# Kernel optimization log

Hardware: AMD Instinct MI355X
Metric: run time of the kernel (lower is better)

## Reference

```python
import jax, jax.numpy as jnp
import numpy as np

G = 4            # GroupNorm num_groups
EPS_GN = 1e-3    # GroupNorm eps
TEMP = 1.0
SCALE = 4.0      # sqrt(prod(out_ks)) with out_ks=(4,4)
OUT_CL = 8


def group_norm(x):
    # torch GroupNorm(4, d, affine=False) applied on (b, d, n*t): stats per (sample, group)
    b, n, t, d = x.shape
    xr = x.reshape(b, n * t, G, d // G)
    mu = xr.mean(axis=(1, 3), keepdims=True)
    var = xr.var(axis=(1, 3), keepdims=True)
    return ((xr - mu) * jax.lax.rsqrt(var + EPS_GN)).reshape(b, n, t, d)


def mlp(x, W1, b1, W2, b2):
    return jax.nn.leaky_relu(x @ W1 + b1) @ W2 + b2


def sq_dist(x, y):
    # squared euclidean distance, expansion form (avoids [.., nq, nk, d] intermediate)
    x2 = jnp.sum(x * x, axis=-1)
    y2 = jnp.sum(y * y, axis=-1)
    return x2[..., :, None] + y2[..., None, :] - 2.0 * jnp.einsum('...qd,...kd->...qk', x, y)


def clamp_pg(x, lo, hi):
    # clamp_preserve_gradients
    return x + jax.lax.stop_gradient(jnp.clip(x, lo, hi) - x)


def min_pair_tril_sum(d, a):
    # sum_{i<j} 2*min(d_i,d_j)*a_i*a_j along last axis.
    # Identical value to the original tril(diagonal=-1)-masked [.., n, n] reduction,
    # computed via sort + suffix-sum in O(n log n) without the 5-D intermediate.
    order = jnp.argsort(d, axis=-1)
    ds = jnp.take_along_axis(d, order, axis=-1)
    as_ = jnp.take_along_axis(a, order, axis=-1)
    suffix = jnp.flip(jnp.cumsum(jnp.flip(as_, -1), axis=-1), -1) - as_
    return jnp.sum(2.0 * ds * as_ * suffix, axis=-1, keepdims=True)


def calc_compactness(mask, in_dens, in_area, in_iner, qcor, kcor):
    densT = jnp.swapaxes(in_dens, -1, -2)
    areaT = jnp.swapaxes(in_area, -1, -2)
    inerT = jnp.swapaxes(in_iner, -1, -2)
    d = mask * densT           # (b, nw, nq, nk)
    a = mask * areaT
    m = d * a
    i = d * inerT
    dist = sq_dist(qcor, kcor)
    newiner = jnp.sum(i, -1, keepdims=True) + jnp.sum(m * dist, -1, keepdims=True)
    refiner = (jnp.sum(m * a, -1, keepdims=True) + min_pair_tril_sum(d, a)) / (2.0 * np.pi)
    return refiner / newiner, newiner


def cluster(af, dens, area, iner, coor, eps=1e-8):
    b, nw, nqn, nkn = af.shape
    af = clamp_pg(af, 1e-5, 0.99999)
    comp, _ = calc_compactness(af, dens, area, iner, coor, coor)   # (b, nw, nqn, 1)
    log_sc = jnp.zeros((b, nw, 1, nkn), af.dtype)
    log_cl, cl_rs = [], []
    for _ in range(OUT_CL - 1):   # small fixed iteration count (greedy cluster picks)
        score = comp[..., 0] * jnp.exp(log_sc)[:, :, 0, :]          # (b, nw, nqn)
        idx = jnp.argmax(score, axis=-1)                            # (b, nw)
        row = jnp.take_along_axis(af, jnp.broadcast_to(idx[:, :, None, None], (b, nw, 1, nkn)), axis=-2)
        log_cl.append(log_sc + jnp.log(row))
        log_sc = log_sc + jnp.log(1.0 - row)
        cl_rs.append(idx)
    sc_lm = jnp.exp(log_sc)                                         # (b, nw, 1, nkn)
    cl_r = jnp.stack(cl_rs, axis=-1)[..., None]                     # (b, nw, OUT_CL-1, 1)
    cl_m = jnp.concatenate([jnp.exp(jnp.concatenate(log_cl, axis=-2)), sc_lm], axis=-2)  # (b,nw,OUT_CL,nkn)
    densT = jnp.swapaxes(dens, -1, -2)
    areaT = jnp.swapaxes(area, -1, -2)
    cd = cl_m * densT
    ca = cl_m * areaT
    cm = cd * ca
    cl_coor = jnp.einsum('bwck,bwkd->bwcd', cm, coor) / (jnp.sum(cm, -1, keepdims=True) + eps)
    cl_area = jnp.sum(ca, -1, keepdims=True)
    cl_mass = jnp.sum(cm, -1, keepdims=True)
    cl_dens = cl_mass / (cl_area + eps)
    cl_comp, cl_iner = calc_compactness(cl_m, dens, area, iner, cl_coor, coor)
    return cl_m, cl_dens, cl_mass, cl_area, cl_iner, cl_coor, cl_comp, cl_r, sc_lm


def setup_inputs() -> dict:
    key = jax.random.key(0)
    ks = jax.random.split(key, 12)
    b, nw, nn, d = 8, 256, 64, 128
    s = 1.0 / np.sqrt(d)
    return {
        'in_f': jax.random.normal(ks[0], (b, nw, nn, d), jnp.float32),
        'in_geo': jax.random.uniform(ks[1], (b, nw, nn, 6), jnp.float32),
        'W1': jax.random.normal(ks[2], (d, d), jnp.float32) * s,
        'b1': jnp.full((d,), 0.1, jnp.float32),
        'W2': jax.random.normal(ks[3], (d, d), jnp.float32) * s,
        'b2': jnp.full((d,), 0.1, jnp.float32),
        'Wfc': jax.random.normal(ks[4], (d, d), jnp.float32) * s,
        'bfc': jnp.zeros((d,), jnp.float32),
        'Wq': jax.random.normal(ks[5], (d, d), jnp.float32) * s,
        'Wv': jax.random.normal(ks[6], (d, d), jnp.float32) * s,
    }


def reference(in_f, in_geo, W1, b1, W2, b2, Wfc, bfc, Wq, Wv):
    dens = in_geo[..., 0:1]
    area = in_geo[..., 2:3]
    iner = in_geo[..., 3:4]
    coor = in_geo[..., 4:6]
    _f = group_norm(in_f)
    f_m = mlp(_f, W1, b1, W2, b2)
    f_v = _f @ Wv
    q = group_norm(_f @ Wq)                                      # to_cl
    scl = TEMP / SCALE / np.sqrt(q.shape[-1])
    af = jax.nn.softmax(-scl * sq_dist(q, q), axis=-1)           # softmin of scaled sq-dists
    af_max = jnp.max(af, -1, keepdims=True)
    af_min = jnp.min(af, -1, keepdims=True)
    af = (af - af_min) / (af_max - af_min + 1e-8)
    (cl_m, cl_dens, cl_mass, cl_area, cl_iner, cl_coor, cl_comp, cl_r, sc_m) = cluster(af, dens, area, iner, coor)
    cl_mm = cl_m / (jnp.sum(cl_m, -1, keepdims=True) + 1e-8)
    cl_f = jnp.einsum('bwck,bwkd->bwcd', cl_mm, in_f)
    cl_f = cl_f + jnp.einsum('bwck,bwkd->bwcd', cl_mm, f_m) + (jnp.einsum('bwck,bwkd->bwcd', cl_mm, f_v) @ Wfc + bfc)
    cl_geo = jnp.concatenate([cl_dens, cl_mass, cl_area, cl_iner, cl_coor], axis=-1)
    return cl_f, cl_m, cl_geo, cl_r, cl_comp, af, sc_m, q
```

## Files before the change

### kernel.cpp

```cpp
#include <hip/hip_runtime.h>

#define TWO_PI_F 6.28318530717958647692f
#define SCL_F    0.02209708691207961f

typedef __attribute__((ext_vector_type(8))) short s16x8;
typedef __attribute__((ext_vector_type(4))) float f32x4;

__device__ __forceinline__ float rlane(float v, int l) {
    return __uint_as_float((unsigned)__builtin_amdgcn_readlane((int)__float_as_uint(v), l));
}

__device__ __forceinline__ unsigned short f2bf(float f) {
    unsigned u = __float_as_uint(f);
    return (unsigned short)((u + 0x7fff + ((u >> 16) & 1)) >> 16);
}
__device__ __forceinline__ float bf2f(unsigned short h) {
    return __uint_as_float(((unsigned)h) << 16);
}

__global__ __launch_bounds__(256) void gn_partial_k(const float* __restrict__ X,
                                                    float* __restrict__ partials)
{
    int t = threadIdx.x;
    int chunk = blockIdx.x;
    int grp = blockIdx.y;
    int b = grp >> 2, g = grp & 3;
    const float* base = X + ((long)b * 16384 + (long)chunk * 256) * 128 + g * 32;
    float s = 0.f, ss = 0.f;
#pragma unroll
    for (int i = 0; i < 8; i++) {
        int rl_ = i * 32 + (t >> 3);
        int c4 = (t & 7) * 4;
        float4 v = *(const float4*)(base + (long)rl_ * 128 + c4);
        s  += v.x + v.y + v.z + v.w;
        ss += v.x * v.x + v.y * v.y + v.z * v.z + v.w * v.w;
    }
    __shared__ float r0[256], r1[256];
    r0[t] = s; r1[t] = ss;
    __syncthreads();
    for (int off = 128; off > 0; off >>= 1) {
        if (t < off) { r0[t] += r0[t + off]; r1[t] += r1[t + off]; }
        __syncthreads();
    }
    if (t == 0) {
        partials[(grp * 64 + chunk) * 2]     = r0[0];
        partials[(grp * 64 + chunk) * 2 + 1] = r1[0];
    }
}

__global__ void gn_final_k(const float* __restrict__ partials, float* __restrict__ stats,
                           int nblk)
{
    int grp = blockIdx.x, t = threadIdx.x;
    float s = 0.f, ss = 0.f;
    for (int i = t; i < nblk; i += 64) {
        s  += partials[(grp * nblk + i) * 2];
        ss += partials[(grp * nblk + i) * 2 + 1];
    }
    for (int off = 1; off < 64; off <<= 1) { s += __shfl_xor(s, off); ss += __shfl_xor(ss, off); }
    if (t == 0) {
        const float N = 524288.0f;
        float mu = s / N;
        float var = ss / N - mu * mu;
        stats[grp * 2]     = mu;
        stats[grp * 2 + 1] = 1.0f / sqrtf(var + 0.001f);
    }
}

__global__ __launch_bounds__(256) void wvf_prep_k(const float* __restrict__ Wv,
                                                  const float* __restrict__ Wfc,
                                                  float* __restrict__ out)
{
    int t = threadIdx.x;
    int rr = t >> 6, cl = t & 63;
    int r = blockIdx.x * 4 + rr;
    float a0 = 0.f, a1 = 0.f;
    for (int k = 0; k < 128; k++) {
        float wv = Wv[r * 128 + k];
        a0 = fmaf(wv, Wfc[k * 128 + cl], a0);
        a1 = fmaf(wv, Wfc[k * 128 + 64 + cl], a1);
    }
    out[r * 128 + cl] = a0;
    out[r * 128 + 64 + cl] = a1;
}

__global__ __launch_bounds__(256) void wsplit_prep_k(const float* __restrict__ W1,
                                                     const float* __restrict__ Wq,
                                                     unsigned short* __restrict__ WThi,
                                                     unsigned short* __restrict__ WTlo)
{
    int idx = blockIdx.x * 256 + threadIdx.x;
    int col = idx >> 7, k = idx & 127;
    float w = (col < 128) ? W1[k * 128 + col] : Wq[k * 128 + (col - 128)];
    unsigned short hb = f2bf(w);
    float hf = bf2f(hb);
    WThi[col * 128 + k] = hb;
    WTlo[col * 128 + k] = f2bf(w - hf);
}

__global__ __launch_bounds__(512, 4) void gemm_mfma_dual(const float* __restrict__ X,
                                                         const unsigned short* __restrict__ WThi,
                                                         const unsigned short* __restrict__ WTlo,
                                                         const float* __restrict__ b1,
                                                         const float* __restrict__ stats,
                                                         float* __restrict__ C1,
                                                         float* __restrict__ C2,
                                                         float* __restrict__ statsout)
{
    __shared__ short sAhi[128 * 40];
    __shared__ short sAlo[128 * 40];
    __shared__ short sBhi[256 * 40];
    __shared__ short sBlo[256 * 40];
    int t = threadIdx.x;
    int wv = t >> 6, lane = t & 63;
    int half = wv >> 2;
    int mrow0 = (wv & 3) * 32;
    long row0 = (long)blockIdx.x * 128;
    int bidx = (int)(row0 >> 14);

    float muv[4], rsv[4];
#pragma unroll
    for (int g = 0; g < 4; g++) {
        muv[g] = stats[(bidx * 4 + g) * 2];
        rsv[g] = stats[(bidx * 4 + g) * 2 + 1];
    }

    f32x4 acc[2][8];
#pragma unroll
    for (int m2 = 0; m2 < 2; m2++)
#pragma unroll
        for (int nt = 0; nt < 8; nt++) acc[m2][nt] = (f32x4){0.f, 0.f, 0.f, 0.f};

    int lr = lane & 15, lk = (lane >> 4) * 8;
    int arow = t >> 2, akq = (t & 3) * 8;
    int bcol = t >> 1, bko = (t & 1) * 16;
    const float* xsrc = X + (row0 + arow) * 128;

    for (int kt = 0; kt < 4; kt++) {
        {
            float mu = muv[kt], rs = rsv[kt];
            float4 x0 = *(const float4*)(xsrc + kt * 32 + akq);
            float4 x1 = *(const float4*)(xsrc + kt * 32 + akq + 4);
            float v[8];
            v[0] = x0.x; v[1] = x0.y; v[2] = x0.z; v[3] = x0.w;
            v[4] = x1.x; v[5] = x1.y; v[6] = x1.z; v[7] = x1.w;
            s16x8 vh, vl;
#pragma unroll
            for (int j = 0; j < 8; j++) {
                float x = (v[j] - mu) * rs;
                unsigned short hb = f2bf(x);
                float hf = bf2f(hb);
                unsigned short lb = f2bf(x - hf);
                vh[j] = (short)hb;
                vl[j] = (short)lb;
            }
            *(s16x8*)&sAhi[arow * 40 + akq] = vh;
            *(s16x8*)&sAlo[arow * 40 + akq] = vl;
        }
        {
            const unsigned short* sh = WThi + bcol * 128 + kt * 32 + bko;
            const unsigned short* sl = WTlo + bcol * 128 + kt * 32 + bko;
            *(s16x8*)&sBhi[bcol * 40 + bko]     = *(const s16x8*)(sh);
            *(s16x8*)&sBhi[bcol * 40 + bko + 8] = *(const s16x8*)(sh + 8);
            *(s16x8*)&sBlo[bcol * 40 + bko]     = *(const s16x8*)(sl);
            *(s16x8*)&sBlo[bcol * 40 + bko + 8] = *(const s16x8*)(sl + 8);
        }
        __syncthreads();
        s16x8 ahi[2], alo[2];
#pragma unroll
        for (int m2 = 0; m2 < 2; m2++) {
            int row = mrow0 + m2 * 16 + lr;
            ahi[m2] = *(const s16x8*)&sAhi[row * 40 + lk];
            alo[m2] = *(const s16x8*)&sAlo[row * 40 + lk];
        }
#pragma unroll
        for (int nt = 0; nt < 8; nt++) {
            int col = half * 128 + nt * 16 + lr;
            s16x8 bhi = *(const s16x8*)&sBhi[col * 40 + lk];
            s16x8 blo = *(const s16x8*)&sBlo[col * 40 + lk];
#pragma unroll
            for (int m2 = 0; m2 < 2; m2++) {
                acc[m2][nt] = __builtin_amdgcn_mfma_f32_16x16x32_bf16(ahi[m2], bhi, acc[m2][nt], 0, 0, 0);
                acc[m2][nt] = __builtin_amdgcn_mfma_f32_16x16x32_bf16(alo[m2], bhi, acc[m2][nt], 0, 0, 0);
                acc[m2][nt] = __builtin_amdgcn_mfma_f32_16x16x32_bf16(ahi[m2], blo, acc[m2][nt], 0, 0, 0);
            }
        }
        __syncthreads();
    }

    int rg4 = (lane >> 4) * 4;
    float* C = half ? C2 : C1;
    float bv[8];
    if (half == 0) {
#pragma unroll
        for (int nt = 0; nt < 8; nt++) bv[nt] = b1[nt * 16 + lr];
    }
#pragma unroll
    for (int m2 = 0; m2 < 2; m2++) {
        long rbase = row0 + mrow0 + m2 * 16 + rg4;
#pragma unroll
        for (int nt = 0; nt < 8; nt++) {
#pragma unroll
            for (int r = 0; r < 4; r++) {
                float v = acc[m2][nt][r];
                if (half == 0) {
                    v += bv[nt];
                    v = (v >= 0.f) ? v : 0.01f * v;
                }
                C[(rbase + r) * 128 + nt * 16 + lr] = v;
            }
        }
    }
    float s4[4] = {0.f, 0.f, 0.f, 0.f}, ss4[4] = {0.f, 0.f, 0.f, 0.f};
    if (half == 1) {
#pragma unroll
        for (int m2 = 0; m2 < 2; m2++)
#pragma unroll
            for (int nt = 0; nt < 8; nt++) {
                int g = nt >> 1;
#pragma unroll
                for (int r = 0; r < 4; r++) {
                    float v = acc[m2][nt][r];
                    s4[g] += v; ss4[g] += v * v;
                }
            }
    }
    __syncthreads();
    float* sRed = (float*)sAhi;
    if (half == 1) {
        int q = t & 255;
#pragma unroll
        for (int g = 0; g < 4; g++) {
            sRed[q * 8 + 2 * g]     = s4[g];
            sRed[q * 8 + 2 * g + 1] = ss4[g];
        }
    }
    __syncthreads();
    if (t < 8) {
        int g = t >> 1, which = t & 1;
        float a2 = 0.f;
        for (int u = 0; u < 256; u++) a2 += sRed[u * 8 + 2 * g + which];
        statsout[((bidx * 4 + g) * 128 + (int)(blockIdx.x & 127)) * 2 + which] = a2;
    }
}

__global__ __launch_bounds__(256, 2) void attn_v2(const float* __restrict__ Qraw,
                                                  const float* __restrict__ stats,
                                                  float* __restrict__ outQ,
                                                  float* __restrict__ outAF)
{
    __shared__ float sQ[2][8192];
    __shared__ float sN[2][64];
    int t = threadIdx.x;
    int wl = t >> 7;
    int tl = t & 127;
    int w = blockIdx.x * 2 + wl;
    int bidx = w >> 8;
    float muv[4], rsv[4];
#pragma unroll
    for (int g = 0; g < 4; g++) {
        muv[g] = stats[(bidx * 4 + g) * 2];
        rsv[g] = stats[(bidx * 4 + g) * 2 + 1];
    }
    {
        int r = tl >> 1, q0 = (tl & 1) * 16;
        int sw = r >> 3;
        const float* src = Qraw + (long)w * 8192 + r * 128 + q0 * 4;
        float* dstG = outQ + (long)w * 8192 + r * 128 + q0 * 4;
#pragma unroll
        for (int q = 0; q < 16; q++) {
            float4 v = *(const float4*)(src + 4 * q);
            int g = (q0 + q) >> 3;
            float mu = muv[g], rs = rsv[g];
            v.x = (v.x - mu) * rs; v.y = (v.y - mu) * rs;
            v.z = (v.z - mu) * rs; v.w = (v.w - mu) * rs;
            *(float4*)(dstG + 4 * q) = v;
            *(float4*)&sQ[wl][r * 128 + 4 * ((q0 + q) ^ sw)] = v;
        }
    }
    __syncthreads();
    if (tl < 64) {
        int r = tl, sw = r >> 3;
        float s = 0.f;
#pragma unroll
        for (int q = 0; q < 32; q++) {
            float4 v = *(const float4*)&sQ[wl][r * 128 + 4 * (q ^ sw)];
            s += v.x * v.x + v.y * v.y + v.z * v.z + v.w * v.w;
        }
        sN[wl][r] = s;
    }
    __syncthreads();
    int ty = tl >> 4, tx = tl & 15;
    float acc[8][4];
#pragma unroll
    for (int i = 0; i < 8; i++)
#pragma unroll
        for (int bb = 0; bb < 4; bb++) acc[i][bb] = 0.f;
    for (int kq = 0; kq < 32; kq++) {
        float4 bf[4];
#pragma unroll
        for (int bb = 0; bb < 4; bb++) {
            int col = tx * 4 + bb;
            bf[bb] = *(const float4*)&sQ[wl][col * 128 + 4 * (kq ^ (col >> 3))];
        }
#pragma unroll
        for (int i = 0; i < 8; i++) {
            int row = ty * 8 + i;
            float4 av = *(const float4*)&sQ[wl][row * 128 + 4 * (kq ^ (row >> 3))];
#pragma unroll
            for (int bb = 0; bb < 4; bb++)
                acc[i][bb] += av.x * bf[bb].x + av.y * bf[bb].y
                            + av.z * bf[bb].z + av.w * bf[bb].w;
        }
    }
    __syncthreads();
    float* sS = &sQ[wl][0];
#pragma unroll
    for (int i = 0; i < 8; i++) {
        int row = ty * 8 + i;
#pragma unroll
        for (int bb = 0; bb < 4; bb++) {
            int col = tx * 4 + bb;
            sS[row * 65 + col] = sN[wl][row] + sN[wl][col] - 2.f * acc[i][bb];
        }
    }
    __syncthreads();
    if (tl < 64) {
        int r = tl;
        float mnS = sS[r * 65];
        for (int j = 1; j < 64; j++) mnS = fminf(mnS, sS[r * 65 + j]);
        float sum = 0.f, pmx = -1.f, pmn = 1e30f;
        for (int j = 0; j < 64; j++) {
            float p = expf(-SCL_F * (sS[r * 65 + j] - mnS));
            sS[r * 65 + j] = p;
            sum += p;
            pmx = fmaxf(pmx, p);
            pmn = fminf(pmn, p);
        }
        float rsum = 1.0f / sum;
        float amn = pmn * rsum, amx = pmx * rsum;
        float dinv = 1.0f / (amx - amn + 1e-8f);
        float* dst = outAF + (long)w * 4096 + r * 64;
        for (int j = 0; j < 64; j += 4) {
            float4 o;
            o.x = (sS[r * 65 + j + 0] * rsum - amn) * dinv;
            o.y = (sS[r * 65 + j + 1] * rsum - amn) * dinv;
            o.z = (sS[r * 65 + j + 2] * rsum - amn) * dinv;
            o.w = (sS[r * 65 + j + 3] * rsum - amn) * dinv;
            *(float4*)(dst + j) = o;
        }
    }
}

__global__ __launch_bounds__(256, 4) void cluster_v3(const float* __restrict__ AF,
                                                     const float* __restrict__ GEO,
                                                     float* __restrict__ oCLM,
                                                     float* __restrict__ oCLR,
                                                     float* __restrict__ oCOMP,
                                                     float* __restrict__ oGEO,
                                                     float* __restrict__ oSCM,
                                                     float* __restrict__ wCLMM)
{
    __shared__ float sAF[64 * 65];
    __shared__ float sPart[4 * 64 * 3];
    __shared__ float sCLM[8 * 65];
    int t = threadIdx.x, w = blockIdx.x;
    int wv = t >> 6, lane = t & 63;
    const float* afw = AF + (long)w * 4096;
#pragma unroll
    for (int i = 0; i < 4; i++) {
        int f4 = i * 256 + t;
        float4 v = *(const float4*)(afw + f4 * 4);
        int r = f4 >> 4, c4 = (f4 & 15) * 4;
        float* dst = &sAF[r * 65 + c4];
        dst[0] = fminf(fmaxf(v.x, 1e-5f), 0.99999f);
        dst[1] = fminf(fmaxf(v.y, 1e-5f), 0.99999f);
        dst[2] = fminf(fmaxf(v.z, 1e-5f), 0.99999f);
        dst[3] = fminf(fmaxf(v.w, 1e-5f), 0.99999f);
    }
    const float* gp = GEO + ((long)w * 64 + lane) * 6;
    float2 g01 = *(const float2*)(gp);
    float2 g23 = *(const float2*)(gp + 2);
    float2 g45 = *(const float2*)(gp + 4);
    float gD = g01.x, gA = g23.x, gI = g23.y, gX = g45.x, gY = g45.y;
    __syncthreads();

    const float* afrow = &sAF[lane * 65];
    float dk[16], ak[16], T[16];
    float v0 = 0.f, v1 = 0.f;
#pragma unroll
    for (int kk = 0; kk < 16; kk++) {
        int kc = kk * 4 + wv;
        float afk = afrow[kc];
        float d = afk * rlane(gD, kc);
        float a = afk * rlane(gA, kc);
        dk[kk] = d; ak[kk] = a; T[kk] = 0.f;
        float m = d * a;
        float dx = gX - rlane(gX, kc), dy = gY - rlane(gY, kc);
        v0 += d * rlane(gI, kc) + m * (dx * dx + dy * dy);
        v1 += m * a;
    }
    for (int jq = 0; jq < 16; jq++) {
        float dj[4], aj[4];
#pragma unroll
        for (int jr = 0; jr < 4; jr++) {
            int j = jq * 4 + jr;
            float afj = afrow[j];
            dj[jr] = afj * rlane(gD, j);
            aj[jr] = afj * rlane(gA, j);
        }
#pragma unroll
        for (int kk = 0; kk < 16; kk++) {
            if (kk > jq) {
#pragma unroll
                for (int jr = 0; jr < 4; jr++)
                    T[kk] = fmaf(aj[jr], fminf(dj[jr], dk[kk]), T[kk]);
            } else if (kk == jq) {
                if (0 < wv) T[kk] = fmaf(aj[0], fminf(dj[0], dk[kk]), T[kk]);
                if (1 < wv) T[kk] = fmaf(aj[1], fminf(dj[1], dk[kk]), T[kk]);
                if (2 < wv) T[kk] = fmaf(aj[2], fminf(dj[2], dk[kk]), T[kk]);
            }
        }
    }
    float S = 0.f;
#pragma unroll
    for (int kk = 0; kk < 16; kk++) S = fmaf(ak[kk], T[kk], S);
    {
        float* p = &sPart[(wv * 64 + lane) * 3];
        p[0] = v0; p[1] = v1; p[2] = S;
    }
    __syncthreads();

    if (t < 64) {
        int k = lane;
        float c0 = 0.f, c1 = 0.f, c2 = 0.f;
#pragma unroll
        for (int u = 0; u < 4; u++) {
            const float* p = &sPart[(u * 64 + k) * 3];
            c0 += p[0]; c1 += p[1]; c2 += p[2];
        }
        float compk = ((c1 + 2.f * c2) / TWO_PI_F) / c0;
        float sc = 1.0f;
        for (int c = 0; c < 7; c++) {
            float score = compk * sc;
            float mx = score;
            for (int off = 1; off < 64; off <<= 1) mx = fmaxf(mx, __shfl_xor(mx, off));
            unsigned long long bl = __ballot(score == mx);
            int idx = __ffsll(bl) - 1;
            float rowk = sAF[idx * 65 + k];
            float clm = sc * rowk;
            sCLM[c * 65 + k] = clm;
            oCLM[(long)w * 512 + c * 64 + k] = clm;
            if (k == 0) oCLR[(long)w * 7 + c] = (float)idx;
            sc *= (1.0f - rowk);
        }
        sCLM[7 * 65 + k] = sc;
        oCLM[(long)w * 512 + 448 + k] = sc;
        oSCM[(long)w * 64 + k] = sc;
    }
    __syncthreads();

    {
        int k = lane;
        for (int cc = 0; cc < 2; cc++) {
            int c = wv + cc * 4;
            float clm = sCLM[c * 65 + k];
            float cd = clm * gD, ca = clm * gA;
            float cm = cd * ca;
            float T3 = 0.f;
            for (int j = 0; j < 64; j++)
                T3 = fmaf(rlane(ca, j), fminf(rlane(cd, j), cd), T3);
            float r0 = cm, r1 = ca, r2c = cm * gX, r3 = cm * gY, r4 = clm;
            float r5 = cm * ca;
            float r6 = ca * T3 - ca * ca * cd;
            for (int off = 1; off < 64; off <<= 1) {
                r0 += __shfl_xor(r0, off); r1 += __shfl_xor(r1, off);
                r2c += __shfl_xor(r2c, off); r3 += __shfl_xor(r3, off);
                r4 += __shfl_xor(r4, off); r5 += __shfl_xor(r5, off);
                r6 += __shfl_xor(r6, off);
            }
            float mass = r0, area = r1;
            float qx = r2c / (mass + 1e-8f), qy = r3 / (mass + 1e-8f);
            wCLMM[(long)w * 512 + c * 64 + k] = clm / (r4 + 1e-8f);
            float dx = qx - gX, dy = qy - gY;
            float w0v = cd * gI + cm * (dx * dx + dy * dy);
            for (int off = 1; off < 64; off <<= 1) w0v += __shfl_xor(w0v, off);
            if (k == 0) {
                oCOMP[(long)w * 8 + c] = ((r5 + r6) / TWO_PI_F) / w0v;
                float* og = oGEO + (long)w * 48 + c * 6;
                og[0] = mass / (area + 1e-8f); og[1] = mass; og[2] = area;
                og[3] = w0v; og[4] = qx; og[5] = qy;
            }
        }
    }
}

__global__ __launch_bounds__(256, 4) void final_v3(const float* __restrict__ inF,
                                                   const float* __restrict__ H1,
                                                   const float* __restrict__ CLMM,
                                                   const float* __restrict__ stats1,
                                                   const float* __restrict__ W2,
                                                   const float* __restrict__ b2,
                                                   const float* __restrict__ Wvf,
                                                   const float* __restrict__ bfc,
                                                   float* __restrict__ oCLF)
{
    __shared__ float sU[8 * 129];
    __shared__ float sT[8 * 129];
    __shared__ float sP[8 * 129];
    int t = threadIdx.x, w = blockIdx.x;
    int bidx = w >> 8;
    int wv = t >> 6, lane = t & 63;
    int ch = lane + 64 * (wv & 1);

    float mmL[8];
#pragma unroll
    for (int c = 0; c < 8; c++)
        mmL[c] = CLMM[(long)w * 512 + c * 64 + lane];

    float mu = stats1[(bidx * 4 + (ch >> 5)) * 2];
    float rs = stats1[(bidx * 4 + (ch >> 5)) * 2 + 1];

    float acc1[8];
#pragma unroll
    for (int c = 0; c < 8; c++) acc1[c] = 0.f;
    if (wv < 2) {
        const float* src = H1 + (long)w * 8192 + ch;
#pragma unroll 4
        for (int j = 0; j < 64; j++) {
            float f = src[j * 128];
#pragma unroll
            for (int c = 0; c < 8; c++)
                acc1[c] = fmaf(rlane(mmL[c], j), f, acc1[c]);
        }
#pragma unroll
        for (int c = 0; c < 8; c++) sU[c * 129 + ch] = acc1[c];
    } else {
        const float* src = inF + (long)w * 8192 + ch;
#pragma unroll 4
        for (int j = 0; j < 64; j++) {
            float f = (src[j * 128] - mu) * rs;
#pragma unroll
            for (int c = 0; c < 8; c++)
                acc1[c] = fmaf(rlane(mmL[c], j), f, acc1[c]);
        }
#pragma unroll
        for (int c = 0; c < 8; c++) sT[c * 129 + ch] = acc1[c];
    }
    __syncthreads();
    float xL0[8], xL1[8];
    {
        const float* s2 = (wv < 2) ? sU : sT;
#pragma unroll
        for (int c = 0; c < 8; c++) {
            xL0[c] = s2[c * 129 + lane];
            xL1[c] = s2[c * 129 + 64 + lane];
        }
    }
    const float* Wm = (wv < 2) ? W2 : Wvf;
    float acc2[8];
#pragma unroll
    for (int c = 0; c < 8; c++) acc2[c] = 0.f;
#pragma unroll 2
    for (int k = 0; k < 64; k++) {
        float wk = Wm[k * 128 + ch];
#pragma unroll
        for (int c = 0; c < 8; c++)
            acc2[c] = fmaf(rlane(xL0[c], k), wk, acc2[c]);
    }
#pragma unroll 2
    for (int k = 0; k < 64; k++) {
        float wk = Wm[(k + 64) * 128 + ch];
#pragma unroll
        for (int c = 0; c < 8; c++)
            acc2[c] = fmaf(rlane(xL1[c], k), wk, acc2[c]);
    }
    if (wv >= 2) {
        float sig = 1.0f / rs;
#pragma unroll
        for (int c = 0; c < 8; c++) {
            float t1ch = (wv & 1) ? xL1[c] : xL0[c];
            acc2[c] = fmaf(t1ch, sig, acc2[c]);
        }
#pragma unroll
        for (int c = 0; c < 8; c++) sP[c * 129 + ch] = acc2[c];
    }
    __syncthreads();
    if (wv < 2) {
        float scv[8];
#pragma unroll
        for (int c = 0; c < 8; c++) {
            float s = mmL[c];
            for (int off = 1; off < 64; off <<= 1) s += __shfl_xor(s, off);
            scv[c] = s;
        }
        float mub = mu + b2[ch];
        float bfv = bfc[ch];
#pragma unroll
        for (int c = 0; c < 8; c++) {
            float o = acc2[c] + sP[c * 129 + ch] + scv[c] * mub + bfv;
            oCLF[(long)w * 1024 + c * 128 + ch] = o;
        }
    }
}

extern "C" void kernel_launch(void* const* d_in, const int* in_sizes, int n_in,
                              void* d_out, int out_size, void* d_ws, size_t ws_size,
                              hipStream_t stream)
{
    (void)in_sizes; (void)n_in; (void)out_size; (void)ws_size;
    const float* in_f   = (const float*)d_in[0];
    const float* in_geo = (const float*)d_in[1];
    const float* W1  = (const float*)d_in[2];
    const float* b1  = (const float*)d_in[3];
    const float* W2  = (const float*)d_in[4];
    const float* b2  = (const float*)d_in[5];
    const float* Wfc = (const float*)d_in[6];
    const float* bfc = (const float*)d_in[7];
    const float* Wq  = (const float*)d_in[8];
    const float* Wv  = (const float*)d_in[9];
    float* out = (float*)d_out;
    float* ws  = (float*)d_ws;

    float* qh     = ws;
    float* clmm   = ws + 16777216;
    float* stats1 = ws + 17825792;
    float* stats2 = ws + 17825856;
    float* wvf    = ws + 17825920;
    float* part   = ws + 17842304;

    unsigned short* wthi = (unsigned short*)clmm;
    unsigned short* wtlo = ((unsigned short*)clmm) + 32768;

    float* o_clf  = out;
    float* o_clm  = out + 2097152;
    float* o_geo  = out + 3145728;
    float* o_clr  = out + 3244032;
    float* o_comp = out + 3258368;
    float* o_af   = out + 3274752;
    float* o_scm  = out + 11663360;
    float* o_q    = out + 11794432;

    gn_partial_k<<<dim3(64, 32), 256, 0, stream>>>(in_f, part);
    gn_final_k<<<32, 64, 0, stream>>>(part, stats1, 64);
    wvf_prep_k<<<32, 256, 0, stream>>>(Wv, Wfc, wvf);
    wsplit_prep_k<<<128, 256, 0, stream>>>(W1, Wq, wthi, wtlo);
    gemm_mfma_dual<<<1024, 512, 0, stream>>>(in_f, wthi, wtlo, b1, stats1, qh, o_q, part);
    gn_final_k<<<32, 64, 0, stream>>>(part, stats2, 128);
    attn_v2<<<1024, 256, 0, stream>>>(o_q, stats2, o_q, o_af);
    cluster_v3<<<2048, 256, 0, stream>>>(o_af, in_geo, o_clm, o_clr, o_comp, o_geo,
                                         o_scm, clmm);
    final_v3<<<2048, 256, 0, stream>>>(in_f, qh, clmm, stats1, W2, b2, wvf, bfc, o_clf);
}
```

Before: 394.4 us.

## Rewrite attention kernel with split-bf16 MFMA Gram and parallel softmin

Replaces the FP32 scalar Gram-matrix computation in the attention kernel with bf16 MFMA instructions. Each value is split into a hi and a lo bf16 part and three products are accumulated to keep near-fp32 accuracy. Each block now handles one window with four wavefronts, and the row normalisation and softmin work is spread over four threads per row using shuffles, where only 64 of 128 threads were busy before. The smaller LDS footprint allows three blocks per CU, at the cost of some added precision error from the bf16 split and extra conversion work.

```diff
diff --git a/kernel.cpp b/kernel.cpp
--- a/kernel.cpp
+++ b/kernel.cpp
@@ -244,110 +244,131 @@
     }
 }
 
-__global__ __launch_bounds__(256, 2) void attn_v2(const float* __restrict__ Qraw,
+__global__ __launch_bounds__(256, 3) void attn_v3(const float* __restrict__ Qraw,
                                                   const float* __restrict__ stats,
                                                   float* __restrict__ outQ,
                                                   float* __restrict__ outAF)
 {
-    __shared__ float sQ[2][8192];
-    __shared__ float sN[2][64];
+    __shared__ short sYhi[4 * 64 * 40];
+    __shared__ short sYlo[4 * 64 * 40];
+    __shared__ float sN[64];
+    float* sS = (float*)sYlo;
     int t = threadIdx.x;
-    int wl = t >> 7;
-    int tl = t & 127;
-    int w = blockIdx.x * 2 + wl;
+    int wv = t >> 6, lane = t & 63;
+    int w = blockIdx.x;
     int bidx = w >> 8;
-    float muv[4], rsv[4];
-#pragma unroll
-    for (int g = 0; g < 4; g++) {
-        muv[g] = stats[(bidx * 4 + g) * 2];
-        rsv[g] = stats[(bidx * 4 + g) * 2 + 1];
-    }
+
     {
-        int r = tl >> 1, q0 = (tl & 1) * 16;
-        int sw = r >> 3;
-        const float* src = Qraw + (long)w * 8192 + r * 128 + q0 * 4;
-        float* dstG = outQ + (long)w * 8192 + r * 128 + q0 * 4;
-#pragma unroll
-        for (int q = 0; q < 16; q++) {
-            float4 v = *(const float4*)(src + 4 * q);
-            int g = (q0 + q) >> 3;
-            float mu = muv[g], rs = rsv[g];
-            v.x = (v.x - mu) * rs; v.y = (v.y - mu) * rs;
-            v.z = (v.z - mu) * rs; v.w = (v.w - mu) * rs;
-            *(float4*)(dstG + 4 * q) = v;
-            *(float4*)&sQ[wl][r * 128 + 4 * ((q0 + q) ^ sw)] = v;
-        }
-    }
-    __syncthreads();
-    if (tl < 64) {
-        int r = tl, sw = r >> 3;
-        float s = 0.f;
-#pragma unroll
-        for (int q = 0; q < 32; q++) {
-            float4 v = *(const float4*)&sQ[wl][r * 128 + 4 * (q ^ sw)];
-            s += v.x * v.x + v.y * v.y + v.z * v.z + v.w * v.w;
-        }
-        sN[wl][r] = s;
-    }
-    __syncthreads();
-    int ty = tl >> 4, tx = tl & 15;
-    float acc[8][4];
-#pragma unroll
-    for (int i = 0; i < 8; i++)
-#pragma unroll
-        for (int bb = 0; bb < 4; bb++) acc[i][bb] = 0.f;
-    for (int kq = 0; kq < 32; kq++) {
-        float4 bf[4];
-#pragma unroll
-        for (int bb = 0; bb < 4; bb++) {
-            int col = tx * 4 + bb;
-            bf[bb] = *(const float4*)&sQ[wl][col * 128 + 4 * (kq ^ (col >> 3))];
-        }
-#pragma unroll
-        for (int i = 0; i < 8; i++) {
-            int row = ty * 8 + i;
-            float4 av = *(const float4*)&sQ[wl][row * 128 + 4 * (kq ^ (row >> 3))];
-#pragma unroll
-            for (int bb = 0; bb < 4; bb++)
-                acc[i][bb] += av.x * bf[bb].x + av.y * bf[bb].y
-                            + av.z * bf[bb].z + av.w * bf[bb].w;
-        }
-    }
-    __syncthreads();
-    float* sS = &sQ[wl][0];
-#pragma unroll
-    for (int i = 0; i < 8; i++) {
-        int row = ty * 8 + i;
-#pragma unroll
-        for (int bb = 0; bb < 4; bb++) {
-            int col = tx * 4 + bb;
-            sS[row * 65 + col] = sN[wl][row] + sN[wl][col] - 2.f * acc[i][bb];
-        }
-    }
-    __syncthreads();
-    if (tl < 64) {
-        int r = tl;
-        float mnS = sS[r * 65];
-        for (int j = 1; j < 64; j++) mnS = fminf(mnS, sS[r * 65 + j]);
+        int row = t >> 2, kc = t & 3;
+        float mu = stats[(bidx * 4 + kc) * 2];
+        float rs = stats[(bidx * 4 + kc) * 2 + 1];
+        const float* src = Qraw + (long)w * 8192 + row * 128 + kc * 32;
+        float* dstG = outQ + (long)w * 8192 + row * 128 + kc * 32;
+        s16x8 vh[4], vl[4];
+        float n = 0.f;
+#pragma unroll
+        for (int q4 = 0; q4 < 8; q4++) {
+            float4 v = *(const float4*)(src + 4 * q4);
+            float vv[4] = {v.x, v.y, v.z, v.w};
+            float4 o;
+#pragma unroll
+            for (int e = 0; e < 4; e++) {
+                float x = (vv[e] - mu) * rs;
+                (&o.x)[e] = x;
+                n += x * x;
+                unsigned short hb = f2bf(x);
+                float hf = bf2f(hb);
+                int kk = q4 * 4 + e;
+                vh[kk >> 3][kk & 7] = (short)hb;
+                vl[kk >> 3][kk & 7] = (short)f2bf(x - hf);
+            }
+            *(float4*)(dstG + 4 * q4) = o;
+        }
+        int base = (kc * 64 + row) * 40;
+#pragma unroll
+        for (int u = 0; u < 4; u++) {
+            *(s16x8*)&sYhi[base + u * 8] = vh[u];
+            *(s16x8*)&sYlo[base + u * 8] = vl[u];
+        }
+        n += __shfl_xor(n, 1);
+        n += __shfl_xor(n, 2);
+        if (kc == 0) sN[row] = n;
+    }
+    __syncthreads();
+
+    f32x4 acc[4];
+#pragma unroll
+    for (int nt = 0; nt < 4; nt++) acc[nt] = (f32x4){0.f, 0.f, 0.f, 0.f};
+    int lr = lane & 15, lk = (lane >> 4) * 8;
+    for (int kc = 0; kc < 4; kc++) {
+        int abase = (kc * 64 + wv * 16 + lr) * 40 + lk;
+        s16x8 ahi = *(const s16x8*)&sYhi[abase];
+        s16x8 alo = *(const s16x8*)&sYlo[abase];
+#pragma unroll
+        for (int nt = 0; nt < 4; nt++) {
+            int bbase = (kc * 64 + nt * 16 + lr) * 40 + lk;
+            s16x8 bhi = *(const s16x8*)&sYhi[bbase];
+            s16x8 blo = *(const s16x8*)&sYlo[bbase];
+            acc[nt] = __builtin_amdgcn_mfma_f32_16x16x32_bf16(ahi, bhi, acc[nt], 0, 0, 0);
+            acc[nt] = __builtin_amdgcn_mfma_f32_16x16x32_bf16(alo, bhi, acc[nt], 0, 0, 0);
+            acc[nt] = __builtin_amdgcn_mfma_f32_16x16x32_bf16(ahi, blo, acc[nt], 0, 0, 0);
+        }
+    }
+    __syncthreads();
+
+    {
+        float nrow[4];
+        int r0 = wv * 16 + (lane >> 4) * 4;
+#pragma unroll
+        for (int r = 0; r < 4; r++) nrow[r] = sN[r0 + r];
+#pragma unroll
+        for (int nt = 0; nt < 4; nt++) {
+            float ncol = sN[nt * 16 + lr];
+#pragma unroll
+            for (int r = 0; r < 4; r++)
+                sS[(r0 + r) * 68 + nt * 16 + lr] = nrow[r] + ncol - 2.f * acc[nt][r];
+        }
+    }
+    __syncthreads();
+
+    {
+        int row = t >> 2, j0 = (t & 3) * 16;
+        float p[16];
+#pragma unroll
+        for (int q = 0; q < 4; q++) {
+            float4 v = *(const float4*)&sS[row * 68 + j0 + 4 * q];
+            p[4 * q + 0] = v.x; p[4 * q + 1] = v.y;
+            p[4 * q + 2] = v.z; p[4 * q + 3] = v.w;
+        }
+        float mn = p[0];
+#pragma unroll
+        for (int i = 1; i < 16; i++) mn = fminf(mn, p[i]);
+        mn = fminf(mn, __shfl_xor(mn, 1));
+        mn = fminf(mn, __shfl_xor(mn, 2));
         float sum = 0.f, pmx = -1.f, pmn = 1e30f;
-        for (int j = 0; j < 64; j++) {
-            float p = expf(-SCL_F * (sS[r * 65 + j] - mnS));
-            sS[r * 65 + j] = p;
-            sum += p;
-            pmx = fmaxf(pmx, p);
-            pmn = fminf(pmn, p);
-        }
+#pragma unroll
+        for (int i = 0; i < 16; i++) {
+            float e = expf(-SCL_F * (p[i] - mn));
+            p[i] = e;
+            sum += e;
+            pmx = fmaxf(pmx, e);
+            pmn = fminf(pmn, e);
+        }
+        sum += __shfl_xor(sum, 1); sum += __shfl_xor(sum, 2);
+        pmx = fmaxf(pmx, __shfl_xor(pmx, 1)); pmx = fmaxf(pmx, __shfl_xor(pmx, 2));
+        pmn = fminf(pmn, __shfl_xor(pmn, 1)); pmn = fminf(pmn, __shfl_xor(pmn, 2));
         float rsum = 1.0f / sum;
         float amn = pmn * rsum, amx = pmx * rsum;
         float dinv = 1.0f / (amx - amn + 1e-8f);
-        float* dst = outAF + (long)w * 4096 + r * 64;
-        for (int j = 0; j < 64; j += 4) {
+        float* dst = outAF + (long)w * 4096 + row * 64 + j0;
+#pragma unroll
+        for (int q = 0; q < 4; q++) {
             float4 o;
-            o.x = (sS[r * 65 + j + 0] * rsum - amn) * dinv;
-            o.y = (sS[r * 65 + j + 1] * rsum - amn) * dinv;
-            o.z = (sS[r * 65 + j + 2] * rsum - amn) * dinv;
-            o.w = (sS[r * 65 + j + 3] * rsum - amn) * dinv;
-            *(float4*)(dst + j) = o;
+            o.x = (p[4 * q + 0] * rsum - amn) * dinv;
+            o.y = (p[4 * q + 1] * rsum - amn) * dinv;
+            o.z = (p[4 * q + 2] * rsum - amn) * dinv;
+            o.w = (p[4 * q + 3] * rsum - amn) * dinv;
+            *(float4*)(dst + 4 * q) = o;
         }
     }
 }
@@ -647,7 +668,7 @@
     wsplit_prep_k<<<128, 256, 0, stream>>>(W1, Wq, wthi, wtlo);
     gemm_mfma_dual<<<1024, 512, 0, stream>>>(in_f, wthi, wtlo, b1, stats1, qh, o_q, part);
     gn_final_k<<<32, 64, 0, stream>>>(part, stats2, 128);
-    attn_v2<<<1024, 256, 0, stream>>>(o_q, stats2, o_q, o_af);
+    attn_v3<<<2048, 256, 0, stream>>>(o_q, stats2, o_q, o_af);
     cluster_v3<<<2048, 256, 0, stream>>>(o_af, in_geo, o_clm, o_clr, o_comp, o_geo,
                                          o_scm, clmm);
     final_v3<<<2048, 256, 0, stream>>>(in_f, qh, clmm, stats1, W2, b2, wvf, bfc, o_clf);
```

Measured after the change: 370.0 us. -6.2%, faster.
